# Optimization experiments

Measured on AMD Instinct MI355X. Metric: run time of the kernel, lower is better.

## Reference

```python
import jax, jax.numpy as jnp
import numpy as np

NUM_USER = 50000
NUM_ITEM = 30000
N_NODES = NUM_USER + NUM_ITEM
N_EDGES = 1_000_000
FEAT_DIM = 768
DIM_LATENT = 128
DIM_ID = 64
NEG_SLOPE = 0.01  # F.leaky_relu default


def leaky_relu(x):
    return jnp.where(x >= 0, x, NEG_SLOPE * x)


def l2_normalize(x, eps=1e-12):
    # F.normalize(dim=-1): divide by clamped L2 norm
    n = jnp.sqrt(jnp.sum(x * x, axis=-1, keepdims=True))
    return x / jnp.maximum(n, eps)


def graph_gat(x, W, edge_index, num_nodes):
    """MGAT GraphGAT: x -> x@W, gated inner-product attention, softmax over
    incoming edges per destination node, scatter-add, L2 normalize."""
    x = x @ W                                    # [N, D]
    src = edge_index[0]                          # j (source)
    dst = edge_index[1]                          # i (target)
    x_j = x[src]                                 # [E, D]
    x_i = x[dst]                                 # [E, D]
    inner = jnp.sum(x_i * x_j, axis=-1)          # [E]
    # gate: sigmoid(deg(src)^-0.5 * inner)
    deg = jax.ops.segment_sum(jnp.ones_like(inner), src, num_segments=num_nodes)
    gate = jax.nn.sigmoid(deg[src] ** -0.5 * inner)
    score = inner * gate                         # [E]
    # segment softmax over destination nodes
    smax = jax.ops.segment_max(score, dst, num_segments=num_nodes)
    e = jnp.exp(score - smax[dst])
    denom = jax.ops.segment_sum(e, dst, num_segments=num_nodes)
    alpha = e / (denom[dst] + 1e-16)             # [E]
    out = jax.ops.segment_sum(x_j * alpha[:, None], dst, num_segments=num_nodes)
    return l2_normalize(out)


def setup_inputs() -> dict:
    key = jax.random.key(0)
    ks = jax.random.split(key, 16)

    def xavier(k, shape):
        fan_in, fan_out = shape[0], shape[1]
        std = float(np.sqrt(2.0 / (fan_in + fan_out)))
        return jax.random.normal(k, shape, dtype=jnp.float32) * std

    features = jax.random.normal(ks[0], (NUM_ITEM, FEAT_DIM), dtype=jnp.float32)
    id_embedding = jax.random.normal(ks[1], (N_NODES, DIM_ID), dtype=jnp.float32)
    # edge_index [2, E] with no self-loops (remove_self_loops is then identity)
    src = jax.random.randint(ks[2], (N_EDGES,), 0, N_NODES)
    off = jax.random.randint(ks[3], (N_EDGES,), 1, N_NODES)
    dst = (src + off) % N_NODES
    edge_index = jnp.stack([src, dst]).astype(jnp.int64)

    return {
        "features": features,
        "id_embedding": id_embedding,
        "edge_index": edge_index,
        "preference": xavier(ks[4], (NUM_USER, DIM_LATENT)),
        "mlp_w": xavier(ks[5], (FEAT_DIM, DIM_LATENT)),
        "mlp_b": jnp.zeros((DIM_LATENT,), dtype=jnp.float32),
        "conv1_w": xavier(ks[6], (DIM_LATENT, DIM_LATENT)),
        "lin1_w": xavier(ks[7], (DIM_LATENT, DIM_ID)),
        "lin1_b": jnp.zeros((DIM_ID,), dtype=jnp.float32),
        "g1_w": xavier(ks[8], (DIM_LATENT, DIM_ID)),
        "g1_b": jnp.zeros((DIM_ID,), dtype=jnp.float32),
        "conv2_w": xavier(ks[9], (DIM_ID, DIM_ID)),
        "lin2_w": xavier(ks[10], (DIM_ID, DIM_ID)),
        "lin2_b": jnp.zeros((DIM_ID,), dtype=jnp.float32),
        "g2_w": xavier(ks[11], (DIM_ID, DIM_ID)),
        "g2_b": jnp.zeros((DIM_ID,), dtype=jnp.float32),
    }


def reference(features, id_embedding, edge_index, preference, mlp_w, mlp_b,
              conv1_w, lin1_w, lin1_b, g1_w, g1_b,
              conv2_w, lin2_w, lin2_b, g2_w, g2_b):
    temp_features = jnp.tanh(features @ mlp_w + mlp_b)        # [num_item, dim_latent]
    x = jnp.concatenate([preference, temp_features], axis=0)  # [N, dim_latent]
    x = l2_normalize(x)

    h = leaky_relu(graph_gat(x, conv1_w, edge_index, N_NODES))
    x_hat = leaky_relu(x @ lin1_w + lin1_b) + id_embedding
    x1 = leaky_relu(h @ g1_w + g1_b + x_hat)                  # [N, dim_id]

    h = leaky_relu(graph_gat(x1, conv2_w, edge_index, N_NODES))
    x_hat = leaky_relu(x1 @ lin2_w + lin2_b) + id_embedding
    x2 = leaky_relu(h @ g2_w + g2_b + x_hat)                  # [N, dim_id]

    return jnp.concatenate([x1, x2], axis=1)                  # [N, 2*dim_id]
```

## Files before the change

### kernel.cpp

```cpp
#include <hip/hip_runtime.h>
#include <hip/hip_bf16.h>
#include <math.h>

#define NUM_USER 50000
#define NUM_ITEM 30000
#define N_NODES  80000
#define N_EDGES  1000000
#define FEAT_DIM 768
#define DLAT 128
#define DID  64
#define NEG_SLOPE 0.01f

#define SCAN_NB ((N_NODES + 255) / 256)

__device__ __forceinline__ float leaky(float v) { return v >= 0.f ? v : NEG_SLOPE * v; }

__device__ __forceinline__ float wave_reduce_sum(float v) {
#pragma unroll
    for (int off = 32; off > 0; off >>= 1) v += __shfl_xor(v, off, 64);
    return v;
}

__device__ __forceinline__ unsigned short f2bf(float f) {
    unsigned int u = __float_as_uint(f);
    unsigned int r = u + 0x7fffu + ((u >> 16) & 1u);
    return (unsigned short)(r >> 16);
}
__device__ __forceinline__ float bf2f(unsigned short h) {
    return __uint_as_float(((unsigned int)h) << 16);
}

typedef __attribute__((ext_vector_type(8))) short short8v;
typedef __attribute__((ext_vector_type(4))) float f32x4;

__device__ __forceinline__ void unpack8(int4 v, float* f) {
    unsigned int u;
    u = (unsigned int)v.x; f[0] = __uint_as_float(u << 16); f[1] = __uint_as_float(u & 0xFFFF0000u);
    u = (unsigned int)v.y; f[2] = __uint_as_float(u << 16); f[3] = __uint_as_float(u & 0xFFFF0000u);
    u = (unsigned int)v.z; f[4] = __uint_as_float(u << 16); f[5] = __uint_as_float(u & 0xFFFF0000u);
    u = (unsigned int)v.w; f[6] = __uint_as_float(u << 16); f[7] = __uint_as_float(u & 0xFFFF0000u);
}

__device__ __forceinline__ void split_store8(
    float4 a, float4 b, unsigned short* dh, unsigned short* dl)
{
    float v[8] = {a.x, a.y, a.z, a.w, b.x, b.y, b.z, b.w};
    unsigned int ph[4], pl[4];
#pragma unroll
    for (int i = 0; i < 4; i++) {
        unsigned short h0 = f2bf(v[2*i]),   l0 = f2bf(v[2*i]   - bf2f(h0));
        unsigned short h1 = f2bf(v[2*i+1]), l1 = f2bf(v[2*i+1] - bf2f(h1));
        ph[i] = (unsigned int)h0 | ((unsigned int)h1 << 16);
        pl[i] = (unsigned int)l0 | ((unsigned int)l1 << 16);
    }
    *(int4*)dh = make_int4((int)ph[0], (int)ph[1], (int)ph[2], (int)ph[3]);
    *(int4*)dl = make_int4((int)pl[0], (int)pl[1], (int)pl[2], (int)pl[3]);
}

__device__ __forceinline__ void prep_one(int id, const float* W, int KK, int NN,
                                         unsigned short* Wh, unsigned short* Wl)
{
    int n = id / KK, k = id - n * KK;
    float v = W[(size_t)k * NN + n];
    unsigned short h = f2bf(v);
    Wh[id] = h;
    Wl[id] = f2bf(v - bf2f(h));
}

__global__ __launch_bounds__(256) void wt_prep_all_kernel(
    const float* __restrict__ mlp_w, const float* __restrict__ c1,
    const float* __restrict__ l1, const float* __restrict__ g1,
    const float* __restrict__ c2, const float* __restrict__ l2,
    const float* __restrict__ g2,
    unsigned short* __restrict__ mlpWh, unsigned short* __restrict__ mlpWl,
    unsigned short* __restrict__ wc1h, unsigned short* __restrict__ wc1l,
    unsigned short* __restrict__ wl1h, unsigned short* __restrict__ wl1l,
    unsigned short* __restrict__ wg1h, unsigned short* __restrict__ wg1l,
    unsigned short* __restrict__ wc2h, unsigned short* __restrict__ wc2l,
    unsigned short* __restrict__ wl2h, unsigned short* __restrict__ wl2l,
    unsigned short* __restrict__ wg2h, unsigned short* __restrict__ wg2l)
{
    int id = blockIdx.x * 256 + threadIdx.x;
    if (id < 98304)       prep_one(id,          mlp_w, FEAT_DIM, DLAT, mlpWh, mlpWl);
    else if (id < 114688) prep_one(id - 98304,  c1, DLAT, DLAT, wc1h, wc1l);
    else if (id < 122880) prep_one(id - 114688, l1, DLAT, DID,  wl1h, wl1l);
    else if (id < 131072) prep_one(id - 122880, g1, DLAT, DID,  wg1h, wg1l);
    else if (id < 135168) prep_one(id - 131072, c2, DID,  DID,  wc2h, wc2l);
    else if (id < 139264) prep_one(id - 135168, l2, DID,  DID,  wl2h, wl2l);
    else if (id < 143360) prep_one(id - 139264, g2, DID,  DID,  wg2h, wg2l);
}

template<int K, int NC>
__global__ __launch_bounds__(256) void conv_mfma_kernel(
    const float* __restrict__ X, int ldx,
    const unsigned short* __restrict__ Wth, const unsigned short* __restrict__ Wtl,
    unsigned short* __restrict__ O, int ldo)
{
    constexpr int NW = NC / 64;
    constexpr int MW = 4 / NW;
    constexpr int WROWS = 64 / MW;
    constexpr int MF = WROWS / 16;
    constexpr int KSTEPS = K / 32;
    constexpr int KP = K + 8;

    __shared__ unsigned short sAh[64][KP];
    __shared__ unsigned short sAl[64][KP];

    const int tid = threadIdx.x;
    const int lane = tid & 63;
    const int w = tid >> 6;
    const int wr = w / NW, wc = w % NW;
    const int r0 = blockIdx.x * 64;

#pragma unroll
    for (int it = 0; it < K / 32; it++) {
        int slot = tid + it * 256;
        int row = slot / (K / 8);
        int k8 = (slot % (K / 8)) * 8;
        const float4* p = (const float4*)(X + (size_t)(r0 + row) * ldx + k8);
        split_store8(p[0], p[1], &sAh[row][k8], &sAl[row][k8]);
    }
    __syncthreads();

    f32x4 acc[MF][4];
#pragma unroll
    for (int m = 0; m < MF; m++)
#pragma unroll
        for (int n = 0; n < 4; n++) acc[m][n] = (f32x4){0.f, 0.f, 0.f, 0.f};

#pragma unroll
    for (int ks = 0; ks < KSTEPS; ks++) {
        int klane = ks * 32 + (lane >> 4) * 8;
        short8v ah[MF], al[MF];
#pragma unroll
        for (int m = 0; m < MF; m++) {
            int row = wr * WROWS + m * 16 + (lane & 15);
            ah[m] = *(const short8v*)&sAh[row][klane];
            al[m] = *(const short8v*)&sAl[row][klane];
        }
#pragma unroll
        for (int n = 0; n < 4; n++) {
            int col = wc * 64 + n * 16 + (lane & 15);
            short8v bh = *(const short8v*)(Wth + (size_t)col * K + klane);
            short8v bl = *(const short8v*)(Wtl + (size_t)col * K + klane);
#pragma unroll
            for (int m = 0; m < MF; m++) {
                acc[m][n] = __builtin_amdgcn_mfma_f32_16x16x32_bf16(ah[m], bh, acc[m][n], 0, 0, 0);
                acc[m][n] = __builtin_amdgcn_mfma_f32_16x16x32_bf16(ah[m], bl, acc[m][n], 0, 0, 0);
                acc[m][n] = __builtin_amdgcn_mfma_f32_16x16x32_bf16(al[m], bh, acc[m][n], 0, 0, 0);
            }
        }
    }

#pragma unroll
    for (int m = 0; m < MF; m++) {
        int rbase = r0 + wr * WROWS + m * 16 + (lane >> 4) * 4;
#pragma unroll
        for (int n = 0; n < 4; n++) {
            int col = wc * 64 + n * 16 + (lane & 15);
#pragma unroll
            for (int q = 0; q < 4; q++)
                O[(size_t)(rbase + q) * ldo + col] = f2bf(acc[m][n][q]);
        }
    }
}

template<int K>
__global__ __launch_bounds__(256) void combine_mfma_kernel(
    const float* __restrict__ H, int ldh,
    const float* __restrict__ X, int ldx,
    const unsigned short* __restrict__ Gth, const unsigned short* __restrict__ Gtl,
    const unsigned short* __restrict__ Lth, const unsigned short* __restrict__ Ltl,
    const float* __restrict__ g_b, const float* __restrict__ lin_b,
    const float* __restrict__ id_emb, float* __restrict__ out, int out_off)
{
    constexpr int KSTEPS = K / 32;
    constexpr int KP = K + 8;

    __shared__ unsigned short sHh[64][KP];
    __shared__ unsigned short sHl[64][KP];
    __shared__ unsigned short sXh[64][KP];
    __shared__ unsigned short sXl[64][KP];

    const int tid = threadIdx.x;
    const int lane = tid & 63;
    const int wr = tid >> 6;
    const int r0 = blockIdx.x * 64;

#pragma unroll
    for (int it = 0; it < K / 32; it++) {
        int slot = tid + it * 256;
        int row = slot / (K / 8);
        int k8 = (slot % (K / 8)) * 8;
        const float4* ph = (const float4*)(H + (size_t)(r0 + row) * ldh + k8);
        split_store8(ph[0], ph[1], &sHh[row][k8], &sHl[row][k8]);
        const float4* px = (const float4*)(X + (size_t)(r0 + row) * ldx + k8);
        split_store8(px[0], px[1], &sXh[row][k8], &sXl[row][k8]);
    }
    __syncthreads();

    f32x4 accG[4], accL[4];
#pragma unroll
    for (int n = 0; n < 4; n++) {
        accG[n] = (f32x4){0.f, 0.f, 0.f, 0.f};
        accL[n] = (f32x4){0.f, 0.f, 0.f, 0.f};
    }

#pragma unroll
    for (int ks = 0; ks < KSTEPS; ks++) {
        int klane = ks * 32 + (lane >> 4) * 8;
        int row = wr * 16 + (lane & 15);
        short8v hh = *(const short8v*)&sHh[row][klane];
        short8v hl = *(const short8v*)&sHl[row][klane];
        short8v xh = *(const short8v*)&sXh[row][klane];
        short8v xl = *(const short8v*)&sXl[row][klane];
#pragma unroll
        for (int n = 0; n < 4; n++) {
            int col = n * 16 + (lane & 15);
            short8v gh = *(const short8v*)(Gth + (size_t)col * K + klane);
            short8v gl = *(const short8v*)(Gtl + (size_t)col * K + klane);
            short8v lh = *(const short8v*)(Lth + (size_t)col * K + klane);
            short8v ll = *(const short8v*)(Ltl + (size_t)col * K + klane);
            accG[n] = __builtin_amdgcn_mfma_f32_16x16x32_bf16(hh, gh, accG[n], 0, 0, 0);
            accG[n] = __builtin_amdgcn_mfma_f32_16x16x32_bf16(hh, gl, accG[n], 0, 0, 0);
            accG[n] = __builtin_amdgcn_mfma_f32_16x16x32_bf16(hl, gh, accG[n], 0, 0, 0);
            accL[n] = __builtin_amdgcn_mfma_f32_16x16x32_bf16(xh, lh, accL[n], 0, 0, 0);
            accL[n] = __builtin_amdgcn_mfma_f32_16x16x32_bf16(xh, ll, accL[n], 0, 0, 0);
            accL[n] = __builtin_amdgcn_mfma_f32_16x16x32_bf16(xl, lh, accL[n], 0, 0, 0);
        }
    }

    int rbase = r0 + wr * 16 + (lane >> 4) * 4;
#pragma unroll
    for (int n = 0; n < 4; n++) {
        int col = n * 16 + (lane & 15);
        float gb = g_b[col], lb = lin_b[col];
#pragma unroll
        for (int q = 0; q < 4; q++) {
            int gr = rbase + q;
            float xhv = leaky(accL[n][q] + lb) + id_emb[(size_t)gr * DID + col];
            float v = leaky(accG[n][q] + gb + xhv);
            out[(size_t)gr * (2 * DID) + out_off + col] = v;
        }
    }
}

__global__ __launch_bounds__(256) void mlp_mfma_kernel(
    const float* __restrict__ F,
    const unsigned short* __restrict__ Wh, const unsigned short* __restrict__ Wl,
    const float* __restrict__ bias, float* __restrict__ xout)
{
    __shared__ unsigned short sAh[64][72];
    __shared__ unsigned short sAl[64][72];
    __shared__ unsigned short sWh[128][72];
    __shared__ unsigned short sWlo[128][72];

    const int tid = threadIdx.x;
    const int lane = tid & 63;
    const int w = tid >> 6;
    const int wr = w >> 1, wc = w & 1;
    const int r0 = blockIdx.x * 64;

    f32x4 acc[2][4];
#pragma unroll
    for (int m = 0; m < 2; m++)
#pragma unroll
        for (int n = 0; n < 4; n++) acc[m][n] = (f32x4){0.f, 0.f, 0.f, 0.f};

    for (int kc = 0; kc < FEAT_DIM; kc += 64) {
#pragma unroll
        for (int it = 0; it < 2; it++) {
            int slot = tid + it * 256;
            int row = slot >> 3;
            int k8 = (slot & 7) * 8;
            int gr = r0 + row;
            float4 a = make_float4(0.f, 0.f, 0.f, 0.f), b = a;
            if (gr < NUM_ITEM) {
                const float4* p = (const float4*)(F + (size_t)gr * FEAT_DIM + kc + k8);
                a = p[0]; b = p[1];
            }
            split_store8(a, b, &sAh[row][k8], &sAl[row][k8]);
        }
#pragma unroll
        for (int it = 0; it < 4; it++) {
            int slot = tid + it * 256;
            int n = slot >> 3;
            int k8 = (slot & 7) * 8;
            *(int4*)&sWh[n][k8]  = *(const int4*)(Wh + (size_t)n * FEAT_DIM + kc + k8);
            *(int4*)&sWlo[n][k8] = *(const int4*)(Wl + (size_t)n * FEAT_DIM + kc + k8);
        }
        __syncthreads();

#pragma unroll
        for (int k0 = 0; k0 < 64; k0 += 32) {
            int klane = k0 + (lane >> 4) * 8;
            short8v ah[2], al[2], bh[4], bl[4];
#pragma unroll
            for (int m = 0; m < 2; m++) {
                int row = wr * 32 + m * 16 + (lane & 15);
                ah[m] = *(const short8v*)&sAh[row][klane];
                al[m] = *(const short8v*)&sAl[row][klane];
            }
#pragma unroll
            for (int n = 0; n < 4; n++) {
                int col = wc * 64 + n * 16 + (lane & 15);
                bh[n] = *(const short8v*)&sWh[col][klane];
                bl[n] = *(const short8v*)&sWlo[col][klane];
            }
#pragma unroll
            for (int m = 0; m < 2; m++)
#pragma unroll
                for (int n = 0; n < 4; n++) {
                    acc[m][n] = __builtin_amdgcn_mfma_f32_16x16x32_bf16(ah[m], bh[n], acc[m][n], 0, 0, 0);
                    acc[m][n] = __builtin_amdgcn_mfma_f32_16x16x32_bf16(ah[m], bl[n], acc[m][n], 0, 0, 0);
                    acc[m][n] = __builtin_amdgcn_mfma_f32_16x16x32_bf16(al[m], bh[n], acc[m][n], 0, 0, 0);
                }
        }
        __syncthreads();
    }

#pragma unroll
    for (int m = 0; m < 2; m++) {
        int rbase = r0 + wr * 32 + m * 16 + (lane >> 4) * 4;
#pragma unroll
        for (int n = 0; n < 4; n++) {
            int col = wc * 64 + n * 16 + (lane & 15);
            float bv = bias[col];
#pragma unroll
            for (int q = 0; q < 4; q++) {
                int gr = rbase + q;
                if (gr < NUM_ITEM)
                    xout[(size_t)gr * DLAT + col] = tanhf(acc[m][n][q] + bv);
            }
        }
    }
}

__global__ __launch_bounds__(256) void normcopy_kernel(
    const float* __restrict__ pref, float* __restrict__ x)
{
    int wid = blockIdx.x * 4 + (threadIdx.x >> 6);
    if (wid >= N_NODES) return;
    int lane = threadIdx.x & 63;
    const float* srow = (wid < NUM_USER) ? (pref + (size_t)wid * DLAT)
                                         : (x + (size_t)wid * DLAT);
    float v0 = srow[lane], v1 = srow[lane + 64];
    float s = wave_reduce_sum(v0 * v0 + v1 * v1);
    float inv = 1.0f / fmaxf(sqrtf(s), 1e-12f);
    float* drow = x + (size_t)wid * DLAT;
    drow[lane] = v0 * inv;
    drow[lane + 64] = v1 * inv;
}

__global__ __launch_bounds__(256) void count_kernel(
    const int* __restrict__ src, const int* __restrict__ dst,
    int* __restrict__ deg_out, int* __restrict__ cnt_in)
{
    int e = blockIdx.x * 256 + threadIdx.x;
    if (e < N_EDGES) {
        atomicAdd(&deg_out[src[e]], 1);
        atomicAdd(&cnt_in[dst[e]], 1);
    }
}

__global__ __launch_bounds__(256) void scan_local_kernel(
    const int* __restrict__ cnt, int* __restrict__ rowptr, int* __restrict__ blocksum)
{
    __shared__ int wsum[4];
    int gid = blockIdx.x * 256 + threadIdx.x;
    int lane = threadIdx.x & 63, w = threadIdx.x >> 6;
    int orig = (gid < N_NODES) ? cnt[gid] : 0;
    int v = orig;
#pragma unroll
    for (int off = 1; off < 64; off <<= 1) {
        int u = __shfl_up(v, off, 64);
        if (lane >= off) v += u;
    }
    if (lane == 63) wsum[w] = v;
    __syncthreads();
    int woff = 0;
#pragma unroll
    for (int i = 0; i < 4; i++) woff += (i < w) ? wsum[i] : 0;
    if (gid < N_NODES) rowptr[gid] = v - orig + woff;
    if (threadIdx.x == 255) blocksum[blockIdx.x] = woff + v;
}

__global__ __launch_bounds__(512) void scan_blocksums_kernel(int* __restrict__ blocksum)
{
    __shared__ int s[512];
    int t = threadIdx.x;
    int orig = (t < SCAN_NB) ? blocksum[t] : 0;
    s[t] = orig;
    __syncthreads();
    for (int off = 1; off < 512; off <<= 1) {
        int u = (t >= off) ? s[t - off] : 0;
        __syncthreads();
        s[t] += u;
        __syncthreads();
    }
    if (t < SCAN_NB) blocksum[t] = s[t] - orig;
}

__global__ __launch_bounds__(256) void scan_add_plus_kernel(
    int* __restrict__ rowptr, const int* __restrict__ blocksum,
    int* __restrict__ cnt, const int* __restrict__ deg_out, float* __restrict__ rsq)
{
    int gid = blockIdx.x * 256 + threadIdx.x;
    if (gid < N_NODES) {
        rowptr[gid] += blocksum[blockIdx.x];
        cnt[gid] = 0;
        rsq[gid] = rsqrtf((float)deg_out[gid]);
    }
    if (gid == 0) rowptr[N_NODES] = N_EDGES;
}

__global__ __launch_bounds__(256) void csr_fill_kernel(
    const int* __restrict__ src, const int* __restrict__ dst,
    const int* __restrict__ rowptr, int* __restrict__ cursor, int* __restrict__ csr_src)
{
    int e = blockIdx.x * 256 + threadIdx.x;
    if (e < N_EDGES) {
        int d = dst[e];
        int slot = rowptr[d] + atomicAdd(&cursor[d], 1);
        csr_src[slot] = src[e];
    }
}

template<int D>
__global__ __launch_bounds__(256) void gat_layer_kernel(
    const unsigned short* __restrict__ xw, const int* __restrict__ rowptr,
    const int* __restrict__ csr_src, const float* __restrict__ rsq_deg,
    float* __restrict__ h)
{
    constexpr int SG  = D / 8;
    constexpr int EPC = 64 / SG;
    int wid = blockIdx.x * 4 + (threadIdx.x >> 6);
    if (wid >= N_NODES) return;
    const int lane = threadIdx.x & 63;
    const int g = lane / SG;
    const int t = lane % SG;
    const int start = rowptr[wid], end = rowptr[wid + 1];

    float xd[8];
    {
        int4 v = *(const int4*)(xw + (size_t)wid * D + 8 * t);
        unpack8(v, xd);
    }

    float m = -1e30f, l = 0.f;
    float acc[8];
#pragma unroll
    for (int c = 0; c < 8; c++) acc[c] = 0.f;

    for (int base = start; base < end; base += EPC) {
        int i = base + g;
        bool valid = (i < end);
        int s = valid ? csr_src[i] : 0;
        int4 av = *(const int4*)(xw + (size_t)s * D + 8 * t);
        float a[8];
        unpack8(av, a);
        float p = a[0]*xd[0] + a[1]*xd[1] + a[2]*xd[2] + a[3]*xd[3]
                + a[4]*xd[4] + a[5]*xd[5] + a[6]*xd[6] + a[7]*xd[7];
#pragma unroll
        for (int off = SG / 2; off > 0; off >>= 1) p += __shfl_xor(p, off, 64);
        float rsd = valid ? rsq_deg[s] : 1.f;
        float gate = 1.0f / (1.0f + __expf(-(p * rsd)));
        float sc = valid ? p * gate : -1e30f;
        float mnew = fmaxf(m, sc);
        float scale = __expf(m - mnew);
        float w = valid ? __expf(sc - mnew) : 0.f;
        l = l * scale + w;
#pragma unroll
        for (int c = 0; c < 8; c++) acc[c] = acc[c] * scale + w * a[c];
        m = mnew;
    }

#pragma unroll
    for (int off = SG; off < 64; off <<= 1) {
        float mo = __shfl_xor(m, off, 64);
        float lo = __shfl_xor(l, off, 64);
        float mnew = fmaxf(m, mo);
        float s1 = __expf(m - mnew), s2 = __expf(mo - mnew);
        l = l * s1 + lo * s2;
#pragma unroll
        for (int c = 0; c < 8; c++) {
            float ao = __shfl_xor(acc[c], off, 64);
            acc[c] = acc[c] * s1 + ao * s2;
        }
        m = mnew;
    }

    float invl = 1.0f / (l + 1e-16f);
    float ss = 0.f;
#pragma unroll
    for (int c = 0; c < 8; c++) { acc[c] *= invl; ss += acc[c] * acc[c]; }
#pragma unroll
    for (int off = SG / 2; off > 0; off >>= 1) ss += __shfl_xor(ss, off, 64);
    float inv = 1.0f / fmaxf(sqrtf(ss), 1e-12f);

    if (g == 0) {
        float4 o0, o1;
        o0.x = leaky(acc[0] * inv); o0.y = leaky(acc[1] * inv);
        o0.z = leaky(acc[2] * inv); o0.w = leaky(acc[3] * inv);
        o1.x = leaky(acc[4] * inv); o1.y = leaky(acc[5] * inv);
        o1.z = leaky(acc[6] * inv); o1.w = leaky(acc[7] * inv);
        float* op = h + (size_t)wid * D + 8 * t;
        *(float4*)(op) = o0;
        *(float4*)(op + 4) = o1;
    }
}

extern "C" void kernel_launch(void* const* d_in, const int* in_sizes, int n_in,
                              void* d_out, int out_size, void* d_ws, size_t ws_size,
                              hipStream_t stream)
{
    const float* features = (const float*)d_in[0];
    const float* id_emb   = (const float*)d_in[1];
    const int*   ei       = (const int*)d_in[2];
    const float* pref     = (const float*)d_in[3];
    const float* mlp_w    = (const float*)d_in[4];
    const float* mlp_b    = (const float*)d_in[5];
    const float* conv1_w  = (const float*)d_in[6];
    const float* lin1_w   = (const float*)d_in[7];
    const float* lin1_b   = (const float*)d_in[8];
    const float* g1_w     = (const float*)d_in[9];
    const float* g1_b     = (const float*)d_in[10];
    const float* conv2_w  = (const float*)d_in[11];
    const float* lin2_w   = (const float*)d_in[12];
    const float* lin2_b   = (const float*)d_in[13];
    const float* g2_w     = (const float*)d_in[14];
    const float* g2_b     = (const float*)d_in[15];
    const int* src = ei;
    const int* dst = ei + N_EDGES;
    float* out = (float*)d_out;

    float* x        = (float*)d_ws;
    unsigned short* xwb = (unsigned short*)(x + (size_t)N_NODES * DLAT);
    float* gat      = (float*)(xwb + (size_t)N_NODES * DLAT);
    int*   deg_out  = (int*)(gat + (size_t)N_NODES * DLAT);
    int*   cnt      = deg_out + N_NODES;
    int*   rowptr   = cnt + N_NODES;
    int*   csr_src  = rowptr + N_NODES + 1;
    int*   blocksum = csr_src + N_EDGES;
    float* rsq_deg  = (float*)(blocksum + SCAN_NB);
    unsigned short* mlpWh = (unsigned short*)gat;
    unsigned short* mlpWl = mlpWh + (size_t)FEAT_DIM * DLAT;
    unsigned short* wbase = (unsigned short*)(
        (((uintptr_t)(rsq_deg + N_NODES)) + 15) & ~(uintptr_t)15);
    unsigned short* wc1h = wbase;
    unsigned short* wc1l = wc1h + 16384;
    unsigned short* wl1h = wc1l + 16384;
    unsigned short* wl1l = wl1h + 8192;
    unsigned short* wg1h = wl1l + 8192;
    unsigned short* wg1l = wg1h + 8192;
    unsigned short* wc2h = wg1l + 8192;
    unsigned short* wc2l = wc2h + 4096;
    unsigned short* wl2h = wc2l + 4096;
    unsigned short* wl2l = wl2h + 4096;
    unsigned short* wg2h = wl2l + 4096;
    unsigned short* wg2l = wg2h + 4096;

    hipMemsetAsync(deg_out, 0, 2 * N_NODES * sizeof(int), stream);
    wt_prep_all_kernel<<<560, 256, 0, stream>>>(
        mlp_w, conv1_w, lin1_w, g1_w, conv2_w, lin2_w, g2_w,
        mlpWh, mlpWl, wc1h, wc1l, wl1h, wl1l, wg1h, wg1l,
        wc2h, wc2l, wl2h, wl2l, wg2h, wg2l);

    count_kernel<<<(N_EDGES + 255) / 256, 256, 0, stream>>>(src, dst, deg_out, cnt);
    scan_local_kernel<<<SCAN_NB, 256, 0, stream>>>(cnt, rowptr, blocksum);
    scan_blocksums_kernel<<<1, 512, 0, stream>>>(blocksum);
    scan_add_plus_kernel<<<SCAN_NB, 256, 0, stream>>>(rowptr, blocksum, cnt, deg_out, rsq_deg);
    csr_fill_kernel<<<(N_EDGES + 255) / 256, 256, 0, stream>>>(src, dst, rowptr, cnt, csr_src);

    mlp_mfma_kernel<<<(NUM_ITEM + 63) / 64, 256, 0, stream>>>(
        features, mlpWh, mlpWl, mlp_b, x + (size_t)NUM_USER * DLAT);
    normcopy_kernel<<<(N_NODES + 3) / 4, 256, 0, stream>>>(pref, x);

    conv_mfma_kernel<DLAT, DLAT><<<N_NODES / 64, 256, 0, stream>>>(
        x, DLAT, wc1h, wc1l, xwb, DLAT);
    gat_layer_kernel<DLAT><<<(N_NODES + 3) / 4, 256, 0, stream>>>(
        xwb, rowptr, csr_src, rsq_deg, gat);
    combine_mfma_kernel<DLAT><<<N_NODES / 64, 256, 0, stream>>>(
        gat, DLAT, x, DLAT, wg1h, wg1l, wl1h, wl1l, g1_b, lin1_b, id_emb, out, 0);

    conv_mfma_kernel<DID, DID><<<N_NODES / 64, 256, 0, stream>>>(
        out, 2 * DID, wc2h, wc2l, xwb, DID);
    gat_layer_kernel<DID><<<(N_NODES + 3) / 4, 256, 0, stream>>>(
        xwb, rowptr, csr_src, rsq_deg, gat);
    combine_mfma_kernel<DID><<<N_NODES / 64, 256, 0, stream>>>(
        gat, DID, out, 2 * DID, wg2h, wg2l, wl2h, wl2l, g2_b, lin2_b, id_emb, out, DID);
}
```

Baseline: 488.7 us.

## Horizontally fuse independent preprocessing kernels into shared launches via block-index dispatch

```diff
diff --git a/kernel.cpp b/kernel.cpp
--- a/kernel.cpp
+++ b/kernel.cpp
@@ -12,6 +12,11 @@
 #define NEG_SLOPE 0.01f
 
 #define SCAN_NB ((N_NODES + 255) / 256)
+#define NB_COUNT ((N_EDGES + 255) / 256)
+#define NB_WT 560
+#define NB_MLP ((NUM_ITEM + 63) / 64)
+#define NB_NORM (N_NODES / 8)
+#define NB_CONV1 (N_NODES / 64)
 
 __device__ __forceinline__ float leaky(float v) { return v >= 0.f ? v : NEG_SLOPE * v; }
 
@@ -57,6 +62,7 @@
     *(int4*)dl = make_int4((int)pl[0], (int)pl[1], (int)pl[2], (int)pl[3]);
 }
 
+
 __device__ __forceinline__ void prep_one(int id, const float* W, int KK, int NN,
                                          unsigned short* Wh, unsigned short* Wl)
 {
@@ -67,7 +73,269 @@
     Wl[id] = f2bf(v - bf2f(h));
 }
 
-__global__ __launch_bounds__(256) void wt_prep_all_kernel(
+__device__ void wt_prep_body(int pb,
+    const float* mlp_w, const float* c1, const float* l1, const float* g1,
+    const float* c2, const float* l2, const float* g2,
+    unsigned short* mlpWh, unsigned short* mlpWl,
+    unsigned short* wc1h, unsigned short* wc1l,
+    unsigned short* wl1h, unsigned short* wl1l,
+    unsigned short* wg1h, unsigned short* wg1l,
+    unsigned short* wc2h, unsigned short* wc2l,
+    unsigned short* wl2h, unsigned short* wl2l,
+    unsigned short* wg2h, unsigned short* wg2l)
+{
+    int id = pb * 256 + threadIdx.x;
+    if (id < 98304)       prep_one(id,          mlp_w, FEAT_DIM, DLAT, mlpWh, mlpWl);
+    else if (id < 114688) prep_one(id - 98304,  c1, DLAT, DLAT, wc1h, wc1l);
+    else if (id < 122880) prep_one(id - 114688, l1, DLAT, DID,  wl1h, wl1l);
+    else if (id < 131072) prep_one(id - 122880, g1, DLAT, DID,  wg1h, wg1l);
+    else if (id < 135168) prep_one(id - 131072, c2, DID,  DID,  wc2h, wc2l);
+    else if (id < 139264) prep_one(id - 135168, l2, DID,  DID,  wl2h, wl2l);
+    else if (id < 143360) prep_one(id - 139264, g2, DID,  DID,  wg2h, wg2l);
+}
+
+__device__ void count_body(int pb, const int* src, const int* dst,
+                           int* deg_out, int* cnt_in)
+{
+    int e = pb * 256 + threadIdx.x;
+    if (e < N_EDGES) {
+        atomicAdd(&deg_out[src[e]], 1);
+        atomicAdd(&cnt_in[dst[e]], 1);
+    }
+}
+
+__device__ void scan_local_body(int pb, const int* cnt, int* rowptr, int* blocksum)
+{
+    __shared__ int wsum[4];
+    int gid = pb * 256 + threadIdx.x;
+    int lane = threadIdx.x & 63, w = threadIdx.x >> 6;
+    int orig = (gid < N_NODES) ? cnt[gid] : 0;
+    int v = orig;
+#pragma unroll
+    for (int off = 1; off < 64; off <<= 1) {
+        int u = __shfl_up(v, off, 64);
+        if (lane >= off) v += u;
+    }
+    if (lane == 63) wsum[w] = v;
+    __syncthreads();
+    int woff = 0;
+#pragma unroll
+    for (int i = 0; i < 4; i++) woff += (i < w) ? wsum[i] : 0;
+    if (gid < N_NODES) rowptr[gid] = v - orig + woff;
+    if (threadIdx.x == 255) blocksum[pb] = woff + v;
+}
+
+__device__ void scan_blocksums_body(int* blocksum)
+{
+    __shared__ int s[512];
+    int t = threadIdx.x;
+    int orig = (t < SCAN_NB) ? blocksum[t] : 0;
+    s[t] = orig;
+    __syncthreads();
+    for (int off = 1; off < 512; off <<= 1) {
+        int u = (t >= off) ? s[t - off] : 0;
+        __syncthreads();
+        s[t] += u;
+        __syncthreads();
+    }
+    if (t < SCAN_NB) blocksum[t] = s[t] - orig;
+}
+
+__device__ void scan_add_plus_body(int pb, int* rowptr, const int* blocksum,
+                                   int* cnt, const int* deg_out, float* rsq)
+{
+    int gid = pb * 256 + threadIdx.x;
+    if (gid < N_NODES) {
+        rowptr[gid] += blocksum[pb];
+        cnt[gid] = 0;
+        rsq[gid] = rsqrtf((float)deg_out[gid]);
+    }
+    if (gid == 0) rowptr[N_NODES] = N_EDGES;
+}
+
+__device__ void mlp_body(int pb, const float* F,
+    const unsigned short* Wh, const unsigned short* Wl,
+    const float* bias, float* xout)
+{
+    __shared__ unsigned short sAh[64][72];
+    __shared__ unsigned short sAl[64][72];
+    __shared__ unsigned short sWh[128][72];
+    __shared__ unsigned short sWlo[128][72];
+
+    const int tid = threadIdx.x;
+    const int lane = tid & 63;
+    const int w = tid >> 6;
+    const int wr = w >> 1, wc = w & 1;
+    const int r0 = pb * 64;
+
+    f32x4 acc[2][4];
+#pragma unroll
+    for (int m = 0; m < 2; m++)
+#pragma unroll
+        for (int n = 0; n < 4; n++) acc[m][n] = (f32x4){0.f, 0.f, 0.f, 0.f};
+
+    for (int kc = 0; kc < FEAT_DIM; kc += 64) {
+#pragma unroll
+        for (int it = 0; it < 2; it++) {
+            int slot = tid + it * 256;
+            int row = slot >> 3;
+            int k8 = (slot & 7) * 8;
+            int gr = r0 + row;
+            float4 a = make_float4(0.f, 0.f, 0.f, 0.f), b = a;
+            if (gr < NUM_ITEM) {
+                const float4* p = (const float4*)(F + (size_t)gr * FEAT_DIM + kc + k8);
+                a = p[0]; b = p[1];
+            }
+            split_store8(a, b, &sAh[row][k8], &sAl[row][k8]);
+        }
+#pragma unroll
+        for (int it = 0; it < 4; it++) {
+            int slot = tid + it * 256;
+            int n = slot >> 3;
+            int k8 = (slot & 7) * 8;
+            *(int4*)&sWh[n][k8]  = *(const int4*)(Wh + (size_t)n * FEAT_DIM + kc + k8);
+            *(int4*)&sWlo[n][k8] = *(const int4*)(Wl + (size_t)n * FEAT_DIM + kc + k8);
+        }
+        __syncthreads();
+
+#pragma unroll
+        for (int k0 = 0; k0 < 64; k0 += 32) {
+            int klane = k0 + (lane >> 4) * 8;
+            short8v ah[2], al[2], bh[4], bl[4];
+#pragma unroll
+            for (int m = 0; m < 2; m++) {
+                int row = wr * 32 + m * 16 + (lane & 15);
+                ah[m] = *(const short8v*)&sAh[row][klane];
+                al[m] = *(const short8v*)&sAl[row][klane];
+            }
+#pragma unroll
+            for (int n = 0; n < 4; n++) {
+                int col = wc * 64 + n * 16 + (lane & 15);
+                bh[n] = *(const short8v*)&sWh[col][klane];
+                bl[n] = *(const short8v*)&sWlo[col][klane];
+            }
+#pragma unroll
+            for (int m = 0; m < 2; m++)
+#pragma unroll
+                for (int n = 0; n < 4; n++) {
+                    acc[m][n] = __builtin_amdgcn_mfma_f32_16x16x32_bf16(ah[m], bh[n], acc[m][n], 0, 0, 0);
+                    acc[m][n] = __builtin_amdgcn_mfma_f32_16x16x32_bf16(ah[m], bl[n], acc[m][n], 0, 0, 0);
+                    acc[m][n] = __builtin_amdgcn_mfma_f32_16x16x32_bf16(al[m], bh[n], acc[m][n], 0, 0, 0);
+                }
+        }
+        __syncthreads();
+    }
+
+#pragma unroll
+    for (int m = 0; m < 2; m++) {
+        int rbase = r0 + wr * 32 + m * 16 + (lane >> 4) * 4;
+#pragma unroll
+        for (int n = 0; n < 4; n++) {
+            int col = wc * 64 + n * 16 + (lane & 15);
+            float bv = bias[col];
+#pragma unroll
+            for (int q = 0; q < 4; q++) {
+                int gr = rbase + q;
+                if (gr < NUM_ITEM)
+                    xout[(size_t)gr * DLAT + col] = tanhf(acc[m][n][q] + bv);
+            }
+        }
+    }
+}
+
+__device__ void normcopy_body(int pb, const float* pref, float* x)
+{
+    int wid = pb * 8 + (threadIdx.x >> 6);
+    if (wid >= N_NODES) return;
+    int lane = threadIdx.x & 63;
+    const float* srow = (wid < NUM_USER) ? (pref + (size_t)wid * DLAT)
+                                         : (x + (size_t)wid * DLAT);
+    float v0 = srow[lane], v1 = srow[lane + 64];
+    float s = wave_reduce_sum(v0 * v0 + v1 * v1);
+    float inv = 1.0f / fmaxf(sqrtf(s), 1e-12f);
+    float* drow = x + (size_t)wid * DLAT;
+    drow[lane] = v0 * inv;
+    drow[lane + 64] = v1 * inv;
+}
+
+template<int K, int NC>
+__device__ void conv_body(int pb, const float* X, int ldx,
+    const unsigned short* Wth, const unsigned short* Wtl,
+    unsigned short* O, int ldo)
+{
+    constexpr int NW = NC / 64;
+    constexpr int MW = 4 / NW;
+    constexpr int WROWS = 64 / MW;
+    constexpr int MF = WROWS / 16;
+    constexpr int KSTEPS = K / 32;
+    constexpr int KP = K + 8;
+
+    __shared__ unsigned short sAh[64][KP];
+    __shared__ unsigned short sAl[64][KP];
+
+    const int tid = threadIdx.x;
+    const int lane = tid & 63;
+    const int w = tid >> 6;
+    const int wr = w / NW, wc = w % NW;
+    const int r0 = pb * 64;
+
+#pragma unroll
+    for (int it = 0; it < K / 32; it++) {
+        int slot = tid + it * 256;
+        int row = slot / (K / 8);
+        int k8 = (slot % (K / 8)) * 8;
+        const float4* p = (const float4*)(X + (size_t)(r0 + row) * ldx + k8);
+        split_store8(p[0], p[1], &sAh[row][k8], &sAl[row][k8]);
+    }
+    __syncthreads();
+
+    f32x4 acc[MF][4];
+#pragma unroll
+    for (int m = 0; m < MF; m++)
+#pragma unroll
+        for (int n = 0; n < 4; n++) acc[m][n] = (f32x4){0.f, 0.f, 0.f, 0.f};
+
+#pragma unroll
+    for (int ks = 0; ks < KSTEPS; ks++) {
+        int klane = ks * 32 + (lane >> 4) * 8;
+        short8v ah[MF], al[MF];
+#pragma unroll
+        for (int m = 0; m < MF; m++) {
+            int row = wr * WROWS + m * 16 + (lane & 15);
+            ah[m] = *(const short8v*)&sAh[row][klane];
+            al[m] = *(const short8v*)&sAl[row][klane];
+        }
+#pragma unroll
+        for (int n = 0; n < 4; n++) {
+            int col = wc * 64 + n * 16 + (lane & 15);
+            short8v bh = *(const short8v*)(Wth + (size_t)col * K + klane);
+            short8v bl = *(const short8v*)(Wtl + (size_t)col * K + klane);
+#pragma unroll
+            for (int m = 0; m < MF; m++) {
+                acc[m][n] = __builtin_amdgcn_mfma_f32_16x16x32_bf16(ah[m], bh, acc[m][n], 0, 0, 0);
+                acc[m][n] = __builtin_amdgcn_mfma_f32_16x16x32_bf16(ah[m], bl, acc[m][n], 0, 0, 0);
+                acc[m][n] = __builtin_amdgcn_mfma_f32_16x16x32_bf16(al[m], bh, acc[m][n], 0, 0, 0);
+            }
+        }
+    }
+
+#pragma unroll
+    for (int m = 0; m < MF; m++) {
+        int rbase = r0 + wr * WROWS + m * 16 + (lane >> 4) * 4;
+#pragma unroll
+        for (int n = 0; n < 4; n++) {
+            int col = wc * 64 + n * 16 + (lane & 15);
+#pragma unroll
+            for (int q = 0; q < 4; q++)
+                O[(size_t)(rbase + q) * ldo + col] = f2bf(acc[m][n][q]);
+        }
+    }
+}
+
+
+__global__ __launch_bounds__(256) void k_count_wtprep(
+    const int* __restrict__ src, const int* __restrict__ dst,
+    int* __restrict__ deg_out, int* __restrict__ cnt_in,
     const float* __restrict__ mlp_w, const float* __restrict__ c1,
     const float* __restrict__ l1, const float* __restrict__ g1,
     const float* __restrict__ c2, const float* __restrict__ l2,
@@ -80,88 +348,131 @@
     unsigned short* __restrict__ wl2h, unsigned short* __restrict__ wl2l,
     unsigned short* __restrict__ wg2h, unsigned short* __restrict__ wg2l)
 {
-    int id = blockIdx.x * 256 + threadIdx.x;
-    if (id < 98304)       prep_one(id,          mlp_w, FEAT_DIM, DLAT, mlpWh, mlpWl);
-    else if (id < 114688) prep_one(id - 98304,  c1, DLAT, DLAT, wc1h, wc1l);
-    else if (id < 122880) prep_one(id - 114688, l1, DLAT, DID,  wl1h, wl1l);
-    else if (id < 131072) prep_one(id - 122880, g1, DLAT, DID,  wg1h, wg1l);
-    else if (id < 135168) prep_one(id - 131072, c2, DID,  DID,  wc2h, wc2l);
-    else if (id < 139264) prep_one(id - 135168, l2, DID,  DID,  wl2h, wl2l);
-    else if (id < 143360) prep_one(id - 139264, g2, DID,  DID,  wg2h, wg2l);
-}
-
-template<int K, int NC>
-__global__ __launch_bounds__(256) void conv_mfma_kernel(
+    int b = blockIdx.x;
+    if (b < NB_COUNT) count_body(b, src, dst, deg_out, cnt_in);
+    else wt_prep_body(b - NB_COUNT, mlp_w, c1, l1, g1, c2, l2, g2,
+                      mlpWh, mlpWl, wc1h, wc1l, wl1h, wl1l, wg1h, wg1l,
+                      wc2h, wc2l, wl2h, wl2l, wg2h, wg2l);
+}
+
+__global__ __launch_bounds__(256) void k_scanl_mlp(
+    const int* __restrict__ cnt, int* __restrict__ rowptr, int* __restrict__ blocksum,
+    const float* __restrict__ F, const unsigned short* __restrict__ Wh,
+    const unsigned short* __restrict__ Wl, const float* __restrict__ bias,
+    float* __restrict__ xout)
+{
+    int b = blockIdx.x;
+    if (b < SCAN_NB) scan_local_body(b, cnt, rowptr, blocksum);
+    else mlp_body(b - SCAN_NB, F, Wh, Wl, bias, xout);
+}
+
+__global__ __launch_bounds__(512) void k_scanb_norm(
+    int* __restrict__ blocksum, const float* __restrict__ pref, float* __restrict__ x)
+{
+    int b = blockIdx.x;
+    if (b == 0) scan_blocksums_body(blocksum);
+    else normcopy_body(b - 1, pref, x);
+}
+
+__global__ __launch_bounds__(256) void k_scana_conv1(
+    int* __restrict__ rowptr, const int* __restrict__ blocksum,
+    int* __restrict__ cnt, const int* __restrict__ deg_out, float* __restrict__ rsq,
+    const float* __restrict__ X,
+    const unsigned short* __restrict__ Wth, const unsigned short* __restrict__ Wtl,
+    unsigned short* __restrict__ O)
+{
+    int b = blockIdx.x;
+    if (b < SCAN_NB) scan_add_plus_body(b, rowptr, blocksum, cnt, deg_out, rsq);
+    else conv_body<DLAT, DLAT>(b - SCAN_NB, X, DLAT, Wth, Wtl, O, DLAT);
+}
+
+
+__global__ __launch_bounds__(256) void csr_fill_kernel(
+    const int* __restrict__ src, const int* __restrict__ dst,
+    const int* __restrict__ rowptr, int* __restrict__ cursor, int* __restrict__ csr_src)
+{
+    int e = blockIdx.x * 256 + threadIdx.x;
+    if (e < N_EDGES) {
+        int d = dst[e];
+        int slot = rowptr[d] + atomicAdd(&cursor[d], 1);
+        csr_src[slot] = src[e];
+    }
+}
+
+__global__ __launch_bounds__(256) void conv2_kernel(
     const float* __restrict__ X, int ldx,
     const unsigned short* __restrict__ Wth, const unsigned short* __restrict__ Wtl,
     unsigned short* __restrict__ O, int ldo)
 {
-    constexpr int NW = NC / 64;
-    constexpr int MW = 4 / NW;
-    constexpr int WROWS = 64 / MW;
-    constexpr int MF = WROWS / 16;
-    constexpr int KSTEPS = K / 32;
-    constexpr int KP = K + 8;
-
-    __shared__ unsigned short sAh[64][KP];
-    __shared__ unsigned short sAl[64][KP];
-
-    const int tid = threadIdx.x;
-    const int lane = tid & 63;
-    const int w = tid >> 6;
-    const int wr = w / NW, wc = w % NW;
-    const int r0 = blockIdx.x * 64;
-
-#pragma unroll
-    for (int it = 0; it < K / 32; it++) {
-        int slot = tid + it * 256;
-        int row = slot / (K / 8);
-        int k8 = (slot % (K / 8)) * 8;
-        const float4* p = (const float4*)(X + (size_t)(r0 + row) * ldx + k8);
-        split_store8(p[0], p[1], &sAh[row][k8], &sAl[row][k8]);
-    }
-    __syncthreads();
-
-    f32x4 acc[MF][4];
-#pragma unroll
-    for (int m = 0; m < MF; m++)
-#pragma unroll
-        for (int n = 0; n < 4; n++) acc[m][n] = (f32x4){0.f, 0.f, 0.f, 0.f};
-
-#pragma unroll
-    for (int ks = 0; ks < KSTEPS; ks++) {
-        int klane = ks * 32 + (lane >> 4) * 8;
-        short8v ah[MF], al[MF];
-#pragma unroll
-        for (int m = 0; m < MF; m++) {
-            int row = wr * WROWS + m * 16 + (lane & 15);
-            ah[m] = *(const short8v*)&sAh[row][klane];
-            al[m] = *(const short8v*)&sAl[row][klane];
-        }
-#pragma unroll
-        for (int n = 0; n < 4; n++) {
-            int col = wc * 64 + n * 16 + (lane & 15);
-            short8v bh = *(const short8v*)(Wth + (size_t)col * K + klane);
-            short8v bl = *(const short8v*)(Wtl + (size_t)col * K + klane);
-#pragma unroll
-            for (int m = 0; m < MF; m++) {
-                acc[m][n] = __builtin_amdgcn_mfma_f32_16x16x32_bf16(ah[m], bh, acc[m][n], 0, 0, 0);
-                acc[m][n] = __builtin_amdgcn_mfma_f32_16x16x32_bf16(ah[m], bl, acc[m][n], 0, 0, 0);
-                acc[m][n] = __builtin_amdgcn_mfma_f32_16x16x32_bf16(al[m], bh, acc[m][n], 0, 0, 0);
-            }
-        }
-    }
-
-#pragma unroll
-    for (int m = 0; m < MF; m++) {
-        int rbase = r0 + wr * WROWS + m * 16 + (lane >> 4) * 4;
-#pragma unroll
-        for (int n = 0; n < 4; n++) {
-            int col = wc * 64 + n * 16 + (lane & 15);
-#pragma unroll
-            for (int q = 0; q < 4; q++)
-                O[(size_t)(rbase + q) * ldo + col] = f2bf(acc[m][n][q]);
-        }
+    conv_body<DID, DID>(blockIdx.x, X, ldx, Wth, Wtl, O, ldo);
+}
+
+template<int D>
+__global__ __launch_bounds__(256) void gat_layer_kernel(
+    const unsigned short* __restrict__ xw, const int* __restrict__ rowptr,
+    const int* __restrict__ csr_src, const float* __restrict__ rsq_deg,
+    float* __restrict__ h)
+{
+    constexpr int SG  = D / 8;
+    constexpr int EPC = 64 / SG;
+    int wid = blockIdx.x * 4 + (threadIdx.x >> 6);
+    if (wid >= N_NODES) return;
+    const int lane = threadIdx.x & 63;
+    const int g = lane / SG;
+    const int t = lane % SG;
+    const int start = rowptr[wid], end = rowptr[wid + 1];
+
+    float xd[8];
+    unpack8(*(const int4*)(xw + (size_t)wid * D + 8 * t), xd);
+
+    float l = 0.f;
+    float acc[8];
+#pragma unroll
+    for (int c = 0; c < 8; c++) acc[c] = 0.f;
+
+    for (int base = start; base < end; base += EPC) {
+        int i = base + g;
+        bool valid = (i < end);
+        int s = valid ? csr_src[i] : 0;
+        float a[8];
+        unpack8(*(const int4*)(xw + (size_t)s * D + 8 * t), a);
+        float p = a[0]*xd[0] + a[1]*xd[1] + a[2]*xd[2] + a[3]*xd[3]
+                + a[4]*xd[4] + a[5]*xd[5] + a[6]*xd[6] + a[7]*xd[7];
+#pragma unroll
+        for (int off = SG / 2; off > 0; off >>= 1) p += __shfl_xor(p, off, 64);
+        float rsd = valid ? rsq_deg[s] : 1.f;
+        float gate = 1.0f / (1.0f + __expf(-(p * rsd)));
+        float sc = fminf(p * gate, 80.f);
+        float w = valid ? __expf(sc) : 0.f;
+        l += w;
+#pragma unroll
+        for (int c = 0; c < 8; c++) acc[c] += w * a[c];
+    }
+
+#pragma unroll
+    for (int off = SG; off < 64; off <<= 1) {
+        l += __shfl_xor(l, off, 64);
+#pragma unroll
+        for (int c = 0; c < 8; c++) acc[c] += __shfl_xor(acc[c], off, 64);
+    }
+
+    float invl = 1.0f / (l + 1e-16f);
+    float ss = 0.f;
+#pragma unroll
+    for (int c = 0; c < 8; c++) { acc[c] *= invl; ss += acc[c] * acc[c]; }
+#pragma unroll
+    for (int off = SG / 2; off > 0; off >>= 1) ss += __shfl_xor(ss, off, 64);
+    float inv = 1.0f / fmaxf(sqrtf(ss), 1e-12f);
+
+    if (g == 0) {
+        float4 o0, o1;
+        o0.x = leaky(acc[0] * inv); o0.y = leaky(acc[1] * inv);
+        o0.z = leaky(acc[2] * inv); o0.w = leaky(acc[3] * inv);
+        o1.x = leaky(acc[4] * inv); o1.y = leaky(acc[5] * inv);
+        o1.z = leaky(acc[6] * inv); o1.w = leaky(acc[7] * inv);
+        float* op = h + (size_t)wid * D + 8 * t;
+        *(float4*)(op) = o0;
+        *(float4*)(op + 4) = o1;
     }
 }
 
@@ -242,271 +553,6 @@
             float v = leaky(accG[n][q] + gb + xhv);
             out[(size_t)gr * (2 * DID) + out_off + col] = v;
         }
-    }
-}
-
-__global__ __launch_bounds__(256) void mlp_mfma_kernel(
-    const float* __restrict__ F,
-    const unsigned short* __restrict__ Wh, const unsigned short* __restrict__ Wl,
-    const float* __restrict__ bias, float* __restrict__ xout)
-{
-    __shared__ unsigned short sAh[64][72];
-    __shared__ unsigned short sAl[64][72];
-    __shared__ unsigned short sWh[128][72];
-    __shared__ unsigned short sWlo[128][72];
-
-    const int tid = threadIdx.x;
-    const int lane = tid & 63;
-    const int w = tid >> 6;
-    const int wr = w >> 1, wc = w & 1;
-    const int r0 = blockIdx.x * 64;
-
-    f32x4 acc[2][4];
-#pragma unroll
-    for (int m = 0; m < 2; m++)
-#pragma unroll
-        for (int n = 0; n < 4; n++) acc[m][n] = (f32x4){0.f, 0.f, 0.f, 0.f};
-
-    for (int kc = 0; kc < FEAT_DIM; kc += 64) {
-#pragma unroll
-        for (int it = 0; it < 2; it++) {
-            int slot = tid + it * 256;
-            int row = slot >> 3;
-            int k8 = (slot & 7) * 8;
-            int gr = r0 + row;
-            float4 a = make_float4(0.f, 0.f, 0.f, 0.f), b = a;
-            if (gr < NUM_ITEM) {
-                const float4* p = (const float4*)(F + (size_t)gr * FEAT_DIM + kc + k8);
-                a = p[0]; b = p[1];
-            }
-            split_store8(a, b, &sAh[row][k8], &sAl[row][k8]);
-        }
-#pragma unroll
-        for (int it = 0; it < 4; it++) {
-            int slot = tid + it * 256;
-            int n = slot >> 3;
-            int k8 = (slot & 7) * 8;
-            *(int4*)&sWh[n][k8]  = *(const int4*)(Wh + (size_t)n * FEAT_DIM + kc + k8);
-            *(int4*)&sWlo[n][k8] = *(const int4*)(Wl + (size_t)n * FEAT_DIM + kc + k8);
-        }
-        __syncthreads();
-
-#pragma unroll
-        for (int k0 = 0; k0 < 64; k0 += 32) {
-            int klane = k0 + (lane >> 4) * 8;
-            short8v ah[2], al[2], bh[4], bl[4];
-#pragma unroll
-            for (int m = 0; m < 2; m++) {
-                int row = wr * 32 + m * 16 + (lane & 15);
-                ah[m] = *(const short8v*)&sAh[row][klane];
-                al[m] = *(const short8v*)&sAl[row][klane];
-            }
-#pragma unroll
-            for (int n = 0; n < 4; n++) {
-                int col = wc * 64 + n * 16 + (lane & 15);
-                bh[n] = *(const short8v*)&sWh[col][klane];
-                bl[n] = *(const short8v*)&sWlo[col][klane];
-            }
-#pragma unroll
-            for (int m = 0; m < 2; m++)
-#pragma unroll
-                for (int n = 0; n < 4; n++) {
-                    acc[m][n] = __builtin_amdgcn_mfma_f32_16x16x32_bf16(ah[m], bh[n], acc[m][n], 0, 0, 0);
-                    acc[m][n] = __builtin_amdgcn_mfma_f32_16x16x32_bf16(ah[m], bl[n], acc[m][n], 0, 0, 0);
-                    acc[m][n] = __builtin_amdgcn_mfma_f32_16x16x32_bf16(al[m], bh[n], acc[m][n], 0, 0, 0);
-                }
-        }
-        __syncthreads();
-    }
-
-#pragma unroll
-    for (int m = 0; m < 2; m++) {
-        int rbase = r0 + wr * 32 + m * 16 + (lane >> 4) * 4;
-#pragma unroll
-        for (int n = 0; n < 4; n++) {
-            int col = wc * 64 + n * 16 + (lane & 15);
-            float bv = bias[col];
-#pragma unroll
-            for (int q = 0; q < 4; q++) {
-                int gr = rbase + q;
-                if (gr < NUM_ITEM)
-                    xout[(size_t)gr * DLAT + col] = tanhf(acc[m][n][q] + bv);
-            }
-        }
-    }
-}
-
-__global__ __launch_bounds__(256) void normcopy_kernel(
-    const float* __restrict__ pref, float* __restrict__ x)
-{
-    int wid = blockIdx.x * 4 + (threadIdx.x >> 6);
-    if (wid >= N_NODES) return;
-    int lane = threadIdx.x & 63;
-    const float* srow = (wid < NUM_USER) ? (pref + (size_t)wid * DLAT)
-                                         : (x + (size_t)wid * DLAT);
-    float v0 = srow[lane], v1 = srow[lane + 64];
-    float s = wave_reduce_sum(v0 * v0 + v1 * v1);
-    float inv = 1.0f / fmaxf(sqrtf(s), 1e-12f);
-    float* drow = x + (size_t)wid * DLAT;
-    drow[lane] = v0 * inv;
-    drow[lane + 64] = v1 * inv;
-}
-
-__global__ __launch_bounds__(256) void count_kernel(
-    const int* __restrict__ src, const int* __restrict__ dst,
-    int* __restrict__ deg_out, int* __restrict__ cnt_in)
-{
-    int e = blockIdx.x * 256 + threadIdx.x;
-    if (e < N_EDGES) {
-        atomicAdd(&deg_out[src[e]], 1);
-        atomicAdd(&cnt_in[dst[e]], 1);
-    }
-}
-
-__global__ __launch_bounds__(256) void scan_local_kernel(
-    const int* __restrict__ cnt, int* __restrict__ rowptr, int* __restrict__ blocksum)
-{
-    __shared__ int wsum[4];
-    int gid = blockIdx.x * 256 + threadIdx.x;
-    int lane = threadIdx.x & 63, w = threadIdx.x >> 6;
-    int orig = (gid < N_NODES) ? cnt[gid] : 0;
-    int v = orig;
-#pragma unroll
-    for (int off = 1; off < 64; off <<= 1) {
-        int u = __shfl_up(v, off, 64);
-        if (lane >= off) v += u;
-    }
-    if (lane == 63) wsum[w] = v;
-    __syncthreads();
-    int woff = 0;
-#pragma unroll
-    for (int i = 0; i < 4; i++) woff += (i < w) ? wsum[i] : 0;
-    if (gid < N_NODES) rowptr[gid] = v - orig + woff;
-    if (threadIdx.x == 255) blocksum[blockIdx.x] = woff + v;
-}
-
-__global__ __launch_bounds__(512) void scan_blocksums_kernel(int* __restrict__ blocksum)
-{
-    __shared__ int s[512];
-    int t = threadIdx.x;
-    int orig = (t < SCAN_NB) ? blocksum[t] : 0;
-    s[t] = orig;
-    __syncthreads();
-    for (int off = 1; off < 512; off <<= 1) {
-        int u = (t >= off) ? s[t - off] : 0;
-        __syncthreads();
-        s[t] += u;
-        __syncthreads();
-    }
-    if (t < SCAN_NB) blocksum[t] = s[t] - orig;
-}
-
-__global__ __launch_bounds__(256) void scan_add_plus_kernel(
-    int* __restrict__ rowptr, const int* __restrict__ blocksum,
-    int* __restrict__ cnt, const int* __restrict__ deg_out, float* __restrict__ rsq)
-{
-    int gid = blockIdx.x * 256 + threadIdx.x;
-    if (gid < N_NODES) {
-        rowptr[gid] += blocksum[blockIdx.x];
-        cnt[gid] = 0;
-        rsq[gid] = rsqrtf((float)deg_out[gid]);
-    }
-    if (gid == 0) rowptr[N_NODES] = N_EDGES;
-}
-
-__global__ __launch_bounds__(256) void csr_fill_kernel(
-    const int* __restrict__ src, const int* __restrict__ dst,
-    const int* __restrict__ rowptr, int* __restrict__ cursor, int* __restrict__ csr_src)
-{
-    int e = blockIdx.x * 256 + threadIdx.x;
-    if (e < N_EDGES) {
-        int d = dst[e];
-        int slot = rowptr[d] + atomicAdd(&cursor[d], 1);
-        csr_src[slot] = src[e];
-    }
-}
-
-template<int D>
-__global__ __launch_bounds__(256) void gat_layer_kernel(
-    const unsigned short* __restrict__ xw, const int* __restrict__ rowptr,
-    const int* __restrict__ csr_src, const float* __restrict__ rsq_deg,
-    float* __restrict__ h)
-{
-    constexpr int SG  = D / 8;
-    constexpr int EPC = 64 / SG;
-    int wid = blockIdx.x * 4 + (threadIdx.x >> 6);
-    if (wid >= N_NODES) return;
-    const int lane = threadIdx.x & 63;
-    const int g = lane / SG;
-    const int t = lane % SG;
-    const int start = rowptr[wid], end = rowptr[wid + 1];
-
-    float xd[8];
-    {
-        int4 v = *(const int4*)(xw + (size_t)wid * D + 8 * t);
-        unpack8(v, xd);
-    }
-
-    float m = -1e30f, l = 0.f;
-    float acc[8];
-#pragma unroll
-    for (int c = 0; c < 8; c++) acc[c] = 0.f;
-
-    for (int base = start; base < end; base += EPC) {
-        int i = base + g;
-        bool valid = (i < end);
-        int s = valid ? csr_src[i] : 0;
-        int4 av = *(const int4*)(xw + (size_t)s * D + 8 * t);
-        float a[8];
-        unpack8(av, a);
-        float p = a[0]*xd[0] + a[1]*xd[1] + a[2]*xd[2] + a[3]*xd[3]
-                + a[4]*xd[4] + a[5]*xd[5] + a[6]*xd[6] + a[7]*xd[7];
-#pragma unroll
-        for (int off = SG / 2; off > 0; off >>= 1) p += __shfl_xor(p, off, 64);
-        float rsd = valid ? rsq_deg[s] : 1.f;
-        float gate = 1.0f / (1.0f + __expf(-(p * rsd)));
-        float sc = valid ? p * gate : -1e30f;
-        float mnew = fmaxf(m, sc);
-        float scale = __expf(m - mnew);
-        float w = valid ? __expf(sc - mnew) : 0.f;
-        l = l * scale + w;
-#pragma unroll
-        for (int c = 0; c < 8; c++) acc[c] = acc[c] * scale + w * a[c];
-        m = mnew;
-    }
-
-#pragma unroll
-    for (int off = SG; off < 64; off <<= 1) {
-        float mo = __shfl_xor(m, off, 64);
-        float lo = __shfl_xor(l, off, 64);
-        float mnew = fmaxf(m, mo);
-        float s1 = __expf(m - mnew), s2 = __expf(mo - mnew);
-        l = l * s1 + lo * s2;
-#pragma unroll
-        for (int c = 0; c < 8; c++) {
-            float ao = __shfl_xor(acc[c], off, 64);
-            acc[c] = acc[c] * s1 + ao * s2;
-        }
-        m = mnew;
-    }
-
-    float invl = 1.0f / (l + 1e-16f);
-    float ss = 0.f;
-#pragma unroll
-    for (int c = 0; c < 8; c++) { acc[c] *= invl; ss += acc[c] * acc[c]; }
-#pragma unroll
-    for (int off = SG / 2; off > 0; off >>= 1) ss += __shfl_xor(ss, off, 64);
-    float inv = 1.0f / fmaxf(sqrtf(ss), 1e-12f);
-
-    if (g == 0) {
-        float4 o0, o1;
-        o0.x = leaky(acc[0] * inv); o0.y = leaky(acc[1] * inv);
-        o0.z = leaky(acc[2] * inv); o0.w = leaky(acc[3] * inv);
-        o1.x = leaky(acc[4] * inv); o1.y = leaky(acc[5] * inv);
-        o1.z = leaky(acc[6] * inv); o1.w = leaky(acc[7] * inv);
-        float* op = h + (size_t)wid * D + 8 * t;
-        *(float4*)(op) = o0;
-        *(float4*)(op + 4) = o1;
     }
 }
 
@@ -561,30 +607,30 @@
     unsigned short* wg2l = wg2h + 4096;
 
     hipMemsetAsync(deg_out, 0, 2 * N_NODES * sizeof(int), stream);
-    wt_prep_all_kernel<<<560, 256, 0, stream>>>(
+
+    k_count_wtprep<<<NB_COUNT + NB_WT, 256, 0, stream>>>(
+        src, dst, deg_out, cnt,
         mlp_w, conv1_w, lin1_w, g1_w, conv2_w, lin2_w, g2_w,
         mlpWh, mlpWl, wc1h, wc1l, wl1h, wl1l, wg1h, wg1l,
         wc2h, wc2l, wl2h, wl2l, wg2h, wg2l);
 
-    count_kernel<<<(N_EDGES + 255) / 256, 256, 0, stream>>>(src, dst, deg_out, cnt);
-    scan_local_kernel<<<SCAN_NB, 256, 0, stream>>>(cnt, rowptr, blocksum);
-    scan_blocksums_kernel<<<1, 512, 0, stream>>>(blocksum);
-    scan_add_plus_kernel<<<SCAN_NB, 256, 0, stream>>>(rowptr, blocksum, cnt, deg_out, rsq_deg);
-    csr_fill_kernel<<<(N_EDGES + 255) / 256, 256, 0, stream>>>(src, dst, rowptr, cnt, csr_src);
-
-    mlp_mfma_kernel<<<(NUM_ITEM + 63) / 64, 256, 0, stream>>>(
-        features, mlpWh, mlpWl, mlp_b, x + (size_t)NUM_USER * DLAT);
-    normcopy_kernel<<<(N_NODES + 3) / 4, 256, 0, stream>>>(pref, x);
-
-    conv_mfma_kernel<DLAT, DLAT><<<N_NODES / 64, 256, 0, stream>>>(
-        x, DLAT, wc1h, wc1l, xwb, DLAT);
+    k_scanl_mlp<<<SCAN_NB + NB_MLP, 256, 0, stream>>>(
+        cnt, rowptr, blocksum, features, mlpWh, mlpWl, mlp_b,
+        x + (size_t)NUM_USER * DLAT);
+
+    k_scanb_norm<<<1 + NB_NORM, 512, 0, stream>>>(blocksum, pref, x);
+
+    k_scana_conv1<<<SCAN_NB + NB_CONV1, 256, 0, stream>>>(
+        rowptr, blocksum, cnt, deg_out, rsq_deg, x, wc1h, wc1l, xwb);
+
+    csr_fill_kernel<<<NB_COUNT, 256, 0, stream>>>(src, dst, rowptr, cnt, csr_src);
+
     gat_layer_kernel<DLAT><<<(N_NODES + 3) / 4, 256, 0, stream>>>(
         xwb, rowptr, csr_src, rsq_deg, gat);
     combine_mfma_kernel<DLAT><<<N_NODES / 64, 256, 0, stream>>>(
         gat, DLAT, x, DLAT, wg1h, wg1l, wl1h, wl1l, g1_b, lin1_b, id_emb, out, 0);
 
-    conv_mfma_kernel<DID, DID><<<N_NODES / 64, 256, 0, stream>>>(
-        out, 2 * DID, wc2h, wc2l, xwb, DID);
+    conv2_kernel<<<N_NODES / 64, 256, 0, stream>>>(out, 2 * DID, wc2h, wc2l, xwb, DID);
     gat_layer_kernel<DID><<<(N_NODES + 3) / 4, 256, 0, stream>>>(
         xwb, rowptr, csr_src, rsq_deg, gat);
     combine_mfma_kernel<DID><<<N_NODES / 64, 256, 0, stream>>>(
```

After: 452.7 us. 7.4% less time.
